# Kernel tuning notes

Measured on AMD Instinct MI355X. Metric: run time of the kernel, lower is better.

Reference implementation:

```python
import jax, jax.numpy as jnp
import numpy as np

MAX_SIGMA = [5.0, 5.0, 5.0]
EPS = 1e-7  # K.epsilon()


def _window_sizes():
    # lab2im: windowsize = int32(ceil(2.5 * max_sigma) / 2) * 2 + 1  (odd sizes)
    return (np.int32(np.ceil(2.5 * np.array(MAX_SIGMA)) / 2) * 2 + 1).tolist()


def _gaussian_1d(sigma_i, w):
    # sigma_i: [B, 1], returns normalized gaussian [B, w]
    loc = jnp.arange(w, dtype=jnp.float32) - (w - 1) / 2.0  # [w]
    g = jnp.exp(-(loc[None, :] ** 2) / (2.0 * sigma_i ** 2 + EPS)
                - jnp.log(jnp.sqrt(2.0 * jnp.pi) * sigma_i + EPS))
    return g / jnp.sum(g, axis=-1, keepdims=True)


def _blur(image, sigma):
    # image: [B, D, H, W, C], sigma: [B, n_dims=3]
    B, D, H, W, C = image.shape
    wsizes = _window_sizes()
    # fold batch into channels so the per-sample depthwise conv becomes ONE
    # grouped conv with B*C groups (the fused form the custom kernel targets)
    x = jnp.transpose(image, (1, 2, 3, 0, 4)).reshape(1, D, H, W, B * C)
    for axis, w in enumerate(wsizes):
        g = _gaussian_1d(sigma[:, axis:axis + 1], w)          # [B, w]
        k = jnp.repeat(g, C, axis=0).T                        # [w, B*C] (kernel shared across channels)
        kshape = [w if a == axis else 1 for a in range(3)] + [1, B * C]
        k = k.reshape(kshape)                                 # DHWIO, I=1, O=B*C
        x = jax.lax.conv_general_dilated(
            x, k, window_strides=(1, 1, 1), padding='SAME',
            dimension_numbers=('NDHWC', 'DHWIO', 'NDHWC'),
            feature_group_count=B * C)
    out = x.reshape(D, H, W, B, C)
    return jnp.transpose(out, (3, 0, 1, 2, 4))


def setup_inputs() -> dict:
    key = jax.random.key(0)
    k1, k2 = jax.random.split(key)
    image = jax.random.normal(k1, (4, 160, 160, 160, 2), dtype=jnp.float32)
    sigma = jax.random.uniform(k2, (4, 3), dtype=jnp.float32, minval=0.5, maxval=5.0)
    return {"image": image, "sigma": sigma}


def reference(image, sigma):
    return _blur(image, sigma)
```

## Files before the change

### kernel.cpp

```cpp
#include <hip/hip_runtime.h>
#include <hip/hip_fp16.h>


#define WSZ 13
#define RAD 6
#define SEGA 40
#define NSEGA 4

typedef float nfloat2 __attribute__((ext_vector_type(2)));

constexpr int BB = 4, DD = 160, HH = 160, WW = 160;
constexpr int R2 = 160;
constexpr int P2 = HH * WW;
constexpr int N2 = DD * P2;
constexpr int P4 = P2 / 2;
constexpr int N4 = N2 / 2;
constexpr int NCOL4 = BB * P4;

#define TB 20
#define SLABR (TB + 12)
#define HBS 172

__device__ __forceinline__ void make_weights(float sig, float* w) {
    const float invd = 1.0f / (2.0f * sig * sig + 1e-7f);
    float s = 0.0f;
#pragma unroll
    for (int k = 0; k < WSZ; ++k) {
        const float loc = (float)(k - RAD);
        w[k] = __expf(-loc * loc * invd);
        s += w[k];
    }
    const float inv = 1.0f / s;
#pragma unroll
    for (int k = 0; k < WSZ; ++k) w[k] *= inv;
}

__global__ __launch_bounds__(256) void blur_d(const float2* __restrict__ in,
                                              __half2* __restrict__ ws,
                                              const float* __restrict__ sigma) {
    const float4* in4 = (const float4*)in;
    uint2* wsU = (uint2*)ws;

    const int cid = blockIdx.x * 256 + threadIdx.x;
    const int b   = cid / P4;
    const int rem = cid % P4;

    float wgt[WSZ];
    make_weights(sigma[b * 3 + 0], wgt);

    const int ibase = b * N4 + rem;
    const int obase = b * (N2 / 2) + rem;
    const int p0 = blockIdx.y * SEGA;

    float4 win[WSZ];
#pragma unroll
    for (int k = 0; k < WSZ; ++k) {
        const int q = p0 - RAD + k;
        float4 v = make_float4(0.f, 0.f, 0.f, 0.f);
        if (q >= 0 && q < DD) v = in4[ibase + q * P4];
        win[k] = v;
    }

#pragma unroll 4
    for (int i = 0; i < SEGA; ++i) {
        float ax0 = 0.f, ay0 = 0.f, ax1 = 0.f, ay1 = 0.f;
#pragma unroll
        for (int k = 0; k < WSZ; ++k) {
            const float4 v = win[k];
            ax0 += wgt[k] * v.x; ay0 += wgt[k] * v.y;
            ax1 += wgt[k] * v.z; ay1 += wgt[k] * v.w;
        }
        union { uint2 u; __half2 h[2]; } o;
        o.h[0] = __float22half2_rn(make_float2(ax0, ay0));
        o.h[1] = __float22half2_rn(make_float2(ax1, ay1));
        wsU[obase + (p0 + i) * P4] = o.u;

#pragma unroll
        for (int k = 0; k < WSZ - 1; ++k) win[k] = win[k + 1];
        const int q = p0 + i + RAD + 1;
        float4 v = make_float4(0.f, 0.f, 0.f, 0.f);
        if (q < DD) v = in4[ibase + q * P4];
        win[WSZ - 1] = v;
    }
}

__global__ __launch_bounds__(320) void blur_hw(const __half2* __restrict__ ws,
                                               float2* __restrict__ out,
                                               const float* __restrict__ sigma) {
    __shared__ __align__(16) float2 lds[SLABR * R2];

    const int tid  = threadIdx.x;
    const int bx   = blockIdx.x;
    const int tile = bx & 7;
    const int d    = (bx >> 3) % DD;
    const int b    = bx / (8 * DD);
    const int h0   = tile * TB;

    float wh[WSZ];
    make_weights(sigma[b * 3 + 1], wh);

    const float4* p4 = (const float4*)(ws + b * N2 + d * P2);
#pragma unroll
    for (int j = 0; j < 4; ++j) {
        const int f = j * 320 + tid;
        const int r = f / 40, q = f % 40;
        const int hh = h0 - 6 + r;
        union { float4 f4; __half2 h2[4]; } u;
        u.f4 = make_float4(0.f, 0.f, 0.f, 0.f);
        if (hh >= 0 && hh < HH) u.f4 = p4[hh * 40 + q];
#pragma unroll
        for (int t = 0; t < 4; ++t) lds[r * R2 + q * 4 + t] = __half22float2(u.h2[t]);
    }
    __syncthreads();

    float2 o[10];
    {
        const int w  = tid % 160;
        const int r0 = (tid / 160) * 10;
        float2 win[WSZ];
#pragma unroll
        for (int k = 0; k < WSZ - 1; ++k) win[k] = lds[(r0 + k) * R2 + w];
#pragma unroll
        for (int i = 0; i < 10; ++i) {
            win[WSZ - 1] = lds[(r0 + i + WSZ - 1) * R2 + w];
            float ax = 0.0f, ay = 0.0f;
#pragma unroll
            for (int k = 0; k < WSZ; ++k) { ax += wh[k] * win[k].x; ay += wh[k] * win[k].y; }
            o[i] = make_float2(ax, ay);
#pragma unroll
            for (int k = 0; k < WSZ - 1; ++k) win[k] = win[k + 1];
        }
    }
    __syncthreads();

    float2* hb = lds;
    if (tid < 240) {
        const int r = tid / 12, c = tid % 12;
        const int col = (c < 6) ? c : (160 + c);
        hb[r * HBS + col] = make_float2(0.0f, 0.0f);
    }
    {
        const int w  = tid % 160;
        const int r0 = (tid / 160) * 10;
#pragma unroll
        for (int i = 0; i < 10; ++i) hb[(r0 + i) * HBS + 6 + w] = o[i];
    }
    __syncthreads();

    float ww[WSZ];
    make_weights(sigma[b * 3 + 2], ww);

    nfloat2* oplane = (nfloat2*)(out + b * N2 + d * P2 + h0 * R2);
#pragma unroll
    for (int j = 0; j < 10; ++j) {
        const int oidx = j * 320 + tid;
        const int r = oidx / 160, w = oidx % 160;
        const float2* src = &hb[r * HBS + w];
        float ax = 0.0f, ay = 0.0f;
#pragma unroll
        for (int k = 0; k < WSZ; ++k) { const float2 v = src[k]; ax += ww[k] * v.x; ay += ww[k] * v.y; }
        nfloat2 res; res.x = ax; res.y = ay;
        __builtin_nontemporal_store(res, &oplane[oidx]);
    }
}

extern "C" void kernel_launch(void* const* d_in, const int* in_sizes, int n_in,
                              void* d_out, int out_size, void* d_ws, size_t ws_size,
                              hipStream_t stream) {
    const float2* img   = (const float2*)d_in[0];
    const float*  sigma = (const float*)d_in[1];
    float2*  out = (float2*)d_out;
    __half2* ws  = (__half2*)d_ws;

    blur_d<<<dim3(NCOL4 / 256, NSEGA), dim3(256), 0, stream>>>(img, ws, sigma);
    blur_hw<<<dim3(BB * DD * 8), dim3(320), 0, stream>>>(ws, out, sigma);
}
```

Before: 90.10 us.

## Store LDS slab in fp16 and split depth pass into more segments

```diff
diff --git a/kernel.cpp b/kernel.cpp
--- a/kernel.cpp
+++ b/kernel.cpp
@@ -4,8 +4,8 @@
 
 #define WSZ 13
 #define RAD 6
-#define SEGA 40
-#define NSEGA 4
+#define SEGA 20
+#define NSEGA 8
 
 typedef float nfloat2 __attribute__((ext_vector_type(2)));
 
@@ -49,7 +49,7 @@
     make_weights(sigma[b * 3 + 0], wgt);
 
     const int ibase = b * N4 + rem;
-    const int obase = b * (N2 / 2) + rem;
+    const int obase = b * N4 + rem;
     const int p0 = blockIdx.y * SEGA;
 
     float4 win[WSZ];
@@ -87,7 +87,7 @@
 __global__ __launch_bounds__(320) void blur_hw(const __half2* __restrict__ ws,
                                                float2* __restrict__ out,
                                                const float* __restrict__ sigma) {
-    __shared__ __align__(16) float2 lds[SLABR * R2];
+    __shared__ __align__(16) __half2 lds[SLABR * R2];
 
     const int tid  = threadIdx.x;
     const int bx   = blockIdx.x;
@@ -100,16 +100,15 @@
     make_weights(sigma[b * 3 + 1], wh);
 
     const float4* p4 = (const float4*)(ws + b * N2 + d * P2);
+    float4* l4 = (float4*)lds;
 #pragma unroll
     for (int j = 0; j < 4; ++j) {
         const int f = j * 320 + tid;
         const int r = f / 40, q = f % 40;
         const int hh = h0 - 6 + r;
-        union { float4 f4; __half2 h2[4]; } u;
-        u.f4 = make_float4(0.f, 0.f, 0.f, 0.f);
-        if (hh >= 0 && hh < HH) u.f4 = p4[hh * 40 + q];
-#pragma unroll
-        for (int t = 0; t < 4; ++t) lds[r * R2 + q * 4 + t] = __half22float2(u.h2[t]);
+        float4 v = make_float4(0.f, 0.f, 0.f, 0.f);
+        if (hh >= 0 && hh < HH) v = p4[hh * 40 + q];
+        l4[f] = v;
     }
     __syncthreads();
 
@@ -119,10 +118,10 @@
         const int r0 = (tid / 160) * 10;
         float2 win[WSZ];
 #pragma unroll
-        for (int k = 0; k < WSZ - 1; ++k) win[k] = lds[(r0 + k) * R2 + w];
+        for (int k = 0; k < WSZ - 1; ++k) win[k] = __half22float2(lds[(r0 + k) * R2 + w]);
 #pragma unroll
         for (int i = 0; i < 10; ++i) {
-            win[WSZ - 1] = lds[(r0 + i + WSZ - 1) * R2 + w];
+            win[WSZ - 1] = __half22float2(lds[(r0 + i + WSZ - 1) * R2 + w]);
             float ax = 0.0f, ay = 0.0f;
 #pragma unroll
             for (int k = 0; k < WSZ; ++k) { ax += wh[k] * win[k].x; ay += wh[k] * win[k].y; }
@@ -133,17 +132,17 @@
     }
     __syncthreads();
 
-    float2* hb = lds;
+    __half2* hb = lds;
     if (tid < 240) {
         const int r = tid / 12, c = tid % 12;
         const int col = (c < 6) ? c : (160 + c);
-        hb[r * HBS + col] = make_float2(0.0f, 0.0f);
+        hb[r * HBS + col] = __half2(__float2half(0.f), __float2half(0.f));
     }
     {
         const int w  = tid % 160;
         const int r0 = (tid / 160) * 10;
 #pragma unroll
-        for (int i = 0; i < 10; ++i) hb[(r0 + i) * HBS + 6 + w] = o[i];
+        for (int i = 0; i < 10; ++i) hb[(r0 + i) * HBS + 6 + w] = __float22half2_rn(o[i]);
     }
     __syncthreads();
 
@@ -155,10 +154,13 @@
     for (int j = 0; j < 10; ++j) {
         const int oidx = j * 320 + tid;
         const int r = oidx / 160, w = oidx % 160;
-        const float2* src = &hb[r * HBS + w];
+        const __half2* src = &hb[r * HBS + w];
         float ax = 0.0f, ay = 0.0f;
 #pragma unroll
-        for (int k = 0; k < WSZ; ++k) { const float2 v = src[k]; ax += ww[k] * v.x; ay += ww[k] * v.y; }
+        for (int k = 0; k < WSZ; ++k) {
+            const float2 v = __half22float2(src[k]);
+            ax += ww[k] * v.x; ay += ww[k] * v.y;
+        }
         nfloat2 res; res.x = ax; res.y = ay;
         __builtin_nontemporal_store(res, &oplane[oidx]);
     }
```

Result: slower. 94.14 us (+4.5%).
